# Performance work log

Hardware: AMD Instinct MI355X
Metric: run time of the kernel (lower is better)

## Reference

```python
import jax, jax.numpy as jnp
import numpy as np


def setup_inputs() -> dict:
    key = jax.random.key(0)
    ks = jax.random.split(key, 7)
    B, D, H, M, E = 8192, 512, 512, 50, 3
    return {
        "x": jax.random.normal(ks[0], (B, D), dtype=jnp.float32),
        "mem": jax.random.normal(ks[1], (M, D), dtype=jnp.float32),
        "routing_logits": jax.random.normal(ks[2], (E,), dtype=jnp.float32),
        "proj_W": jax.random.normal(ks[3], (H, D), dtype=jnp.float32) * 0.02,
        "proj_b": jax.random.normal(ks[4], (H,), dtype=jnp.float32) * 0.02,
        "ops_W": jax.random.normal(ks[5], (E, H, H), dtype=jnp.float32) * 0.02,
        "ops_b": jax.random.normal(ks[6], (E, H), dtype=jnp.float32) * 0.02,
    }


def reference(x, mem, routing_logits, proj_W, proj_b, ops_W, ops_b):
    # novelty: mean over (batch, memory) of L2 distance between x rows and memory rows
    diff = x[:, None, :] - mem[None, :, :]                 # [B, M, D] -- dominant memory traffic
    novelty = jnp.minimum(1.5, jnp.mean(jnp.linalg.norm(diff, axis=-1)))

    # top-2 routing over softmax of the (per-module, input-independent) logits
    weights = jax.nn.softmax(routing_logits)
    _, top2 = jax.lax.top_k(weights, 2)
    idx_a, idx_b = top2[0], top2[1]

    # operator = ReLU -> Linear(H, H) -> ReLU (torch Linear: y = x @ W.T + b)
    def op(h, W, b):
        return jax.nn.relu(jnp.einsum("bh,oh->bo", jax.nn.relu(h), W) + b)

    x_proj = jnp.einsum("bd,hd->bh", x, proj_W) + proj_b   # [B, H]
    x1 = op(x_proj, ops_W[idx_a], ops_b[idx_a])
    out = op(x1, ops_W[idx_b], ops_b[idx_b])
    return out, novelty
```

## Files before the change

kernel.cpp:

```cpp
#include <hip/hip_runtime.h>
#include <hip/hip_bf16.h>

typedef _Float16 f16;
typedef _Float16 f16x8 __attribute__((ext_vector_type(8)));
typedef _Float16 f16x4 __attribute__((ext_vector_type(4)));
typedef float f32x4 __attribute__((ext_vector_type(4)));

#define BD 512

__device__ __forceinline__ void llds16(const f16* g, f16* l) {
  __builtin_amdgcn_global_load_lds(
      (const __attribute__((address_space(1))) unsigned int*)g,
      (__attribute__((address_space(3))) unsigned int*)l,
      16, 0, 0);
}

__global__ __launch_bounds__(256) void prep_kernel(
    const float* __restrict__ projW, const float* __restrict__ opsW,
    const float* __restrict__ memf,
    f16* __restrict__ wh,
    f16* __restrict__ memh,
    float* __restrict__ mn2,
    float* __restrict__ novS) {
  const int blk = blockIdx.x;
  if (blk < 1024) {
    int i = blk * 256 + threadIdx.x;
    int e = i * 4;
    const float* s = (e < 262144) ? (projW + e) : (opsW + (e - 262144));
    float4 v = *(const float4*)s;
    f16x4 h;
    h[0] = (f16)v.x; h[1] = (f16)v.y; h[2] = (f16)v.z; h[3] = (f16)v.w;
    *(f16x4*)&wh[e] = h;
  } else {
    const int t = threadIdx.x, l = t & 63, w = t >> 6;
    const int row = (blk - 1024) * 4 + w;
    if (blk == 1024 && t == 0) *novS = 0.0f;
    f16x8 h;
    float ss = 0.0f;
    if (row < 50) {
      const float* src = memf + (size_t)row * BD + l * 8;
      float4 v0 = *(const float4*)src;
      float4 v1 = *(const float4*)(src + 4);
      h[0] = (f16)v0.x; h[1] = (f16)v0.y; h[2] = (f16)v0.z; h[3] = (f16)v0.w;
      h[4] = (f16)v1.x; h[5] = (f16)v1.y; h[6] = (f16)v1.z; h[7] = (f16)v1.w;
      ss = v0.x*v0.x + v0.y*v0.y + v0.z*v0.z + v0.w*v0.w
         + v1.x*v1.x + v1.y*v1.y + v1.z*v1.z + v1.w*v1.w;
      #pragma unroll
      for (int off = 32; off; off >>= 1) ss += __shfl_down(ss, off, 64);
    } else {
      #pragma unroll
      for (int j = 0; j < 8; ++j) h[j] = (f16)0.0f;
    }
    *(f16x8*)&memh[(size_t)row * BD + l * 8] = h;
    if (l == 0) mn2[row] = ss;
  }
}

__global__ __launch_bounds__(256) void conv_nov_kernel(
    const float* __restrict__ x, const f16* __restrict__ memh,
    const float* __restrict__ mn2, f16* __restrict__ xh,
    float* __restrict__ novS) {
  __shared__ __align__(16) f16 As[32 * BD];
  __shared__ float xn[32];
  __shared__ float red[4];
  const int t = threadIdx.x, l = t & 63, w = t >> 6;
  const int rbase = blockIdx.x * 32;

  #pragma unroll
  for (int rr = 0; rr < 8; ++rr) {
    const int r = w * 8 + rr;
    const float* src = x + (size_t)(rbase + r) * BD + l * 8;
    float4 v0 = *(const float4*)src;
    float4 v1 = *(const float4*)(src + 4);
    f16x8 h;
    h[0] = (f16)v0.x; h[1] = (f16)v0.y; h[2] = (f16)v0.z; h[3] = (f16)v0.w;
    h[4] = (f16)v1.x; h[5] = (f16)v1.y; h[6] = (f16)v1.z; h[7] = (f16)v1.w;
    *(f16x8*)&xh[(size_t)(rbase + r) * BD + l * 8] = h;
    const int cs = l ^ (r & 7);
    *(f16x8*)&As[r * BD + cs * 8] = h;
    float ss = v0.x*v0.x + v0.y*v0.y + v0.z*v0.z + v0.w*v0.w
             + v1.x*v1.x + v1.y*v1.y + v1.z*v1.z + v1.w*v1.w;
    #pragma unroll
    for (int off = 32; off; off >>= 1) ss += __shfl_down(ss, off, 64);
    if (l == 0) xn[r] = ss;
  }
  __syncthreads();

  const int lr = l & 15, lk = l >> 4;
  f32x4 acc[2];
  acc[0] = (f32x4){0.f, 0.f, 0.f, 0.f};
  acc[1] = (f32x4){0.f, 0.f, 0.f, 0.f};
  #pragma unroll
  for (int kk = 0; kk < BD; kk += 32) {
    f16x8 b = *(const f16x8*)&memh[(size_t)(w * 16 + lr) * BD + kk + lk * 8];
    #pragma unroll
    for (int m = 0; m < 2; ++m) {
      const int row = m * 16 + lr;
      const int ch = (kk >> 3) + lk;
      f16x8 a = *(const f16x8*)&As[row * BD + ((ch ^ (row & 7)) << 3)];
      acc[m] = __builtin_amdgcn_mfma_f32_16x16x32_f16(a, b, acc[m], 0, 0, 0);
    }
  }
  float local = 0.0f;
  const int mm = w * 16 + lr;
  if (mm < 50) {
    const float mn = mn2[mm];
    #pragma unroll
    for (int m = 0; m < 2; ++m) {
      #pragma unroll
      for (int j = 0; j < 4; ++j) {
        const int row = m * 16 + lk * 4 + j;
        float d = xn[row] - 2.0f * acc[m][j] + mn;
        local += sqrtf(fmaxf(d, 0.0f));
      }
    }
  }
  #pragma unroll
  for (int off = 32; off; off >>= 1) local += __shfl_down(local, off, 64);
  if (l == 0) red[w] = local;
  __syncthreads();
  if (t == 0) atomicAdd(novS, red[0] + red[1] + red[2] + red[3]);
}

template <int PICK, int OUTF16>
__global__ __launch_bounds__(256, 2) void gemm_relu_kernel(
    const f16* __restrict__ A, const f16* __restrict__ Wall,
    const float* __restrict__ ball, const float* __restrict__ logits,
    void* __restrict__ Out, const float* __restrict__ novS,
    float* __restrict__ novOut) {
  __shared__ __align__(16) f16 As[3][4096];
  __shared__ __align__(16) f16 Bs[3][8192];

  const int t = threadIdx.x;
  const int l = t & 63;
  const int w = t >> 6;
  const int wr = w >> 1, wc = w & 1;
  const int lr = l & 15, lk = l >> 4;

  if (PICK == 0 && blockIdx.x == 0 && blockIdx.y == 0 && t == 0)
    novOut[0] = fminf(1.5f, novS[0] * (1.0f / (8192.0f * 50.0f)));

  int widx = 0;
  if (PICK > 0) {
    float l0 = logits[0], l1 = logits[1], l2 = logits[2];
    int ia = 0; float ba = l0;
    if (l1 > ba) { ba = l1; ia = 1; }
    if (l2 > ba) { ba = l2; ia = 2; }
    if (PICK == 1) {
      widx = ia;
    } else {
      int ib = 0; float bb2 = -3.4e38f;
      if (ia != 0 && l0 > bb2) { bb2 = l0; ib = 0; }
      if (ia != 1 && l1 > bb2) { bb2 = l1; ib = 1; }
      if (ia != 2 && l2 > bb2) { bb2 = l2; ib = 2; }
      widx = ib;
    }
  }
  const f16* W = Wall + (size_t)widx * BD * BD;
  const float* bias = ball + widx * BD;

  const int rowBase = blockIdx.x * 64;
  const int colBase = blockIdx.y * 128;

  f32x4 acc[2][4];
  #pragma unroll
  for (int m = 0; m < 2; ++m)
    #pragma unroll
    for (int n = 0; n < 4; ++n) acc[m][n] = (f32x4){0.f, 0.f, 0.f, 0.f};

  auto stage = [&](int buf, int kt) {
    #pragma unroll
    for (int i = 0; i < 2; ++i) {
      const int o = i * 4096 + t * 16;
      const int row = o >> 7;
      const int sch = ((o >> 4) & 7) ^ (row & 7);
      llds16(A + (size_t)(rowBase + row) * BD + kt + sch * 8,
             &As[buf][(i * 4096 + w * 1024) / 2]);
    }
    #pragma unroll
    for (int i = 0; i < 4; ++i) {
      const int o = i * 4096 + t * 16;
      const int row = o >> 7;
      const int sch = ((o >> 4) & 7) ^ (row & 7);
      llds16(W + (size_t)(colBase + row) * BD + kt + sch * 8,
             &Bs[buf][(i * 4096 + w * 1024) / 2]);
    }
  };

  auto compute = [&](int buf) {
    #pragma unroll
    for (int kk = 0; kk < 64; kk += 32) {
      f16x8 af[2], bf[4];
      #pragma unroll
      for (int m = 0; m < 2; ++m) {
        const int row = wr * 32 + m * 16 + lr;
        const int ch = (kk >> 3) + lk;
        af[m] = *(const f16x8*)&As[buf][row * 64 + ((ch ^ (row & 7)) << 3)];
      }
      #pragma unroll
      for (int n = 0; n < 4; ++n) {
        const int row = wc * 64 + n * 16 + lr;
        const int ch = (kk >> 3) + lk;
        bf[n] = *(const f16x8*)&Bs[buf][row * 64 + ((ch ^ (row & 7)) << 3)];
      }
      #pragma unroll
      for (int m = 0; m < 2; ++m)
        #pragma unroll
        for (int n = 0; n < 4; ++n)
          acc[m][n] = __builtin_amdgcn_mfma_f32_16x16x32_f16(af[m], bf[n], acc[m][n], 0, 0, 0);
    }
  };

  stage(0, 0);
  stage(1, 64);
  #pragma unroll
  for (int t8 = 0; t8 < 8; ++t8) {
    if (t8 < 6) stage((t8 + 2) % 3, (t8 + 2) * 64);
    if (t8 <= 5)      asm volatile("s_waitcnt vmcnt(12)" ::: "memory");
    else if (t8 == 6) asm volatile("s_waitcnt vmcnt(6)" ::: "memory");
    else              asm volatile("s_waitcnt vmcnt(0)" ::: "memory");
    __builtin_amdgcn_s_barrier();
    compute(t8 % 3);
    __builtin_amdgcn_s_barrier();
  }

  #pragma unroll
  for (int n = 0; n < 4; ++n) {
    const int col = colBase + wc * 64 + n * 16 + lr;
    const float bb = bias[col];
    #pragma unroll
    for (int m = 0; m < 2; ++m) {
      #pragma unroll
      for (int j = 0; j < 4; ++j) {
        const int rowg = rowBase + wr * 32 + m * 16 + lk * 4 + j;
        float v = acc[m][n][j] + bb;
        v = fmaxf(v, 0.0f);
        if (OUTF16)
          ((f16*)Out)[(size_t)rowg * BD + col] = (f16)v;
        else
          ((float*)Out)[(size_t)rowg * BD + col] = v;
      }
    }
  }
}

extern "C" void kernel_launch(void* const* d_in, const int* in_sizes, int n_in,
                              void* d_out, int out_size, void* d_ws, size_t ws_size,
                              hipStream_t stream) {
  const float* x      = (const float*)d_in[0];
  const float* memf   = (const float*)d_in[1];
  const float* logits = (const float*)d_in[2];
  const float* projW  = (const float*)d_in[3];
  const float* projB  = (const float*)d_in[4];
  const float* opsW   = (const float*)d_in[5];
  const float* opsB   = (const float*)d_in[6];
  float* out = (float*)d_out;

  char* ws = (char*)d_ws;
  f16*   xh   = (f16*)(ws);
  f16*   g0   = (f16*)(ws + 8388608);
  f16*   wh   = (f16*)(ws + 16777216);
  f16*   memh = (f16*)(ws + 18874368);
  float* mn2  = (float*)(ws + 18972672);
  float* novS = (float*)(ws + 18972928);

  prep_kernel<<<1040, 256, 0, stream>>>(projW, opsW, memf, wh, memh, mn2, novS);
  conv_nov_kernel<<<256, 256, 0, stream>>>(x, memh, mn2, xh, novS);

  gemm_relu_kernel<0, 1><<<dim3(128, 4), 256, 0, stream>>>(
      xh, wh, projB, logits, (void*)g0, novS, out + 4194304);
  gemm_relu_kernel<1, 1><<<dim3(128, 4), 256, 0, stream>>>(
      g0, wh + 262144, opsB, logits, (void*)xh, novS, out + 4194304);
  gemm_relu_kernel<2, 0><<<dim3(128, 4), 256, 0, stream>>>(
      xh, wh + 262144, opsB, logits, (void*)out, novS, out + 4194304);
}
```

Before: 49.63 us.

## Fuse weight/memory conversion into novelty kernel and single-barrier GEMM pipeline

Merges the separate prep kernel into the x-conversion/novelty kernel. The weight fp32->fp16 conversion is spread across its 256 blocks, and each block converts memory rows and their norms on the fly instead of reading a precomputed fp16 copy. The global atomic is replaced by per-block partial sums that the first GEMM reduces, which drops one launch and the zero-init dependency. The GEMM main loop moves to one barrier per k-step, issuing the next stage after the barrier and waiting on a tighter vmcnt, and raises priority around the MFMA block. The cost is that every novelty block redundantly reloads and converts the 50 memory rows from fp32.

```diff
diff --git a/kernel.cpp b/kernel.cpp
--- a/kernel.cpp
+++ b/kernel.cpp
@@ -3,7 +3,6 @@
 
 typedef _Float16 f16;
 typedef _Float16 f16x8 __attribute__((ext_vector_type(8)));
-typedef _Float16 f16x4 __attribute__((ext_vector_type(4)));
 typedef float f32x4 __attribute__((ext_vector_type(4)));
 
 #define BD 512
@@ -15,56 +14,32 @@
       16, 0, 0);
 }
 
-__global__ __launch_bounds__(256) void prep_kernel(
+__global__ __launch_bounds__(256) void conv_nov_w_kernel(
+    const float* __restrict__ x, const float* __restrict__ memf,
     const float* __restrict__ projW, const float* __restrict__ opsW,
-    const float* __restrict__ memf,
-    f16* __restrict__ wh,
-    f16* __restrict__ memh,
-    float* __restrict__ mn2,
-    float* __restrict__ novS) {
-  const int blk = blockIdx.x;
-  if (blk < 1024) {
-    int i = blk * 256 + threadIdx.x;
-    int e = i * 4;
-    const float* s = (e < 262144) ? (projW + e) : (opsW + (e - 262144));
-    float4 v = *(const float4*)s;
-    f16x4 h;
-    h[0] = (f16)v.x; h[1] = (f16)v.y; h[2] = (f16)v.z; h[3] = (f16)v.w;
-    *(f16x4*)&wh[e] = h;
-  } else {
-    const int t = threadIdx.x, l = t & 63, w = t >> 6;
-    const int row = (blk - 1024) * 4 + w;
-    if (blk == 1024 && t == 0) *novS = 0.0f;
-    f16x8 h;
-    float ss = 0.0f;
-    if (row < 50) {
-      const float* src = memf + (size_t)row * BD + l * 8;
-      float4 v0 = *(const float4*)src;
-      float4 v1 = *(const float4*)(src + 4);
-      h[0] = (f16)v0.x; h[1] = (f16)v0.y; h[2] = (f16)v0.z; h[3] = (f16)v0.w;
-      h[4] = (f16)v1.x; h[5] = (f16)v1.y; h[6] = (f16)v1.z; h[7] = (f16)v1.w;
-      ss = v0.x*v0.x + v0.y*v0.y + v0.z*v0.z + v0.w*v0.w
-         + v1.x*v1.x + v1.y*v1.y + v1.z*v1.z + v1.w*v1.w;
-      #pragma unroll
-      for (int off = 32; off; off >>= 1) ss += __shfl_down(ss, off, 64);
-    } else {
-      #pragma unroll
-      for (int j = 0; j < 8; ++j) h[j] = (f16)0.0f;
-    }
-    *(f16x8*)&memh[(size_t)row * BD + l * 8] = h;
-    if (l == 0) mn2[row] = ss;
-  }
-}
-
-__global__ __launch_bounds__(256) void conv_nov_kernel(
-    const float* __restrict__ x, const f16* __restrict__ memh,
-    const float* __restrict__ mn2, f16* __restrict__ xh,
-    float* __restrict__ novS) {
+    f16* __restrict__ wh, f16* __restrict__ xh,
+    float* __restrict__ novPart) {
   __shared__ __align__(16) f16 As[32 * BD];
   __shared__ float xn[32];
   __shared__ float red[4];
   const int t = threadIdx.x, l = t & 63, w = t >> 6;
   const int rbase = blockIdx.x * 32;
+
+  {
+    const int e = (blockIdx.x * 256 + t) * 16;
+    const float* s = (e < 262144) ? (projW + e) : (opsW + (e - 262144));
+    float4 v0 = ((const float4*)s)[0];
+    float4 v1 = ((const float4*)s)[1];
+    float4 v2 = ((const float4*)s)[2];
+    float4 v3 = ((const float4*)s)[3];
+    f16x8 h0, h1;
+    h0[0]=(f16)v0.x; h0[1]=(f16)v0.y; h0[2]=(f16)v0.z; h0[3]=(f16)v0.w;
+    h0[4]=(f16)v1.x; h0[5]=(f16)v1.y; h0[6]=(f16)v1.z; h0[7]=(f16)v1.w;
+    h1[0]=(f16)v2.x; h1[1]=(f16)v2.y; h1[2]=(f16)v2.z; h1[3]=(f16)v2.w;
+    h1[4]=(f16)v3.x; h1[5]=(f16)v3.y; h1[6]=(f16)v3.z; h1[7]=(f16)v3.w;
+    *(f16x8*)&wh[e] = h0;
+    *(f16x8*)&wh[e + 8] = h1;
+  }
 
   #pragma unroll
   for (int rr = 0; rr < 8; ++rr) {
@@ -73,8 +48,8 @@
     float4 v0 = *(const float4*)src;
     float4 v1 = *(const float4*)(src + 4);
     f16x8 h;
-    h[0] = (f16)v0.x; h[1] = (f16)v0.y; h[2] = (f16)v0.z; h[3] = (f16)v0.w;
-    h[4] = (f16)v1.x; h[5] = (f16)v1.y; h[6] = (f16)v1.z; h[7] = (f16)v1.w;
+    h[0]=(f16)v0.x; h[1]=(f16)v0.y; h[2]=(f16)v0.z; h[3]=(f16)v0.w;
+    h[4]=(f16)v1.x; h[5]=(f16)v1.y; h[6]=(f16)v1.z; h[7]=(f16)v1.w;
     *(f16x8*)&xh[(size_t)(rbase + r) * BD + l * 8] = h;
     const int cs = l ^ (r & 7);
     *(f16x8*)&As[r * BD + cs * 8] = h;
@@ -87,49 +62,60 @@
   __syncthreads();
 
   const int lr = l & 15, lk = l >> 4;
-  f32x4 acc[2];
-  acc[0] = (f32x4){0.f, 0.f, 0.f, 0.f};
-  acc[1] = (f32x4){0.f, 0.f, 0.f, 0.f};
+  const int mm = w * 16 + lr;
+  f32x4 acc0 = (f32x4){0.f, 0.f, 0.f, 0.f};
+  f32x4 acc1 = (f32x4){0.f, 0.f, 0.f, 0.f};
+  float msq = 0.f;
   #pragma unroll
   for (int kk = 0; kk < BD; kk += 32) {
-    f16x8 b = *(const f16x8*)&memh[(size_t)(w * 16 + lr) * BD + kk + lk * 8];
-    #pragma unroll
-    for (int m = 0; m < 2; ++m) {
-      const int row = m * 16 + lr;
-      const int ch = (kk >> 3) + lk;
-      f16x8 a = *(const f16x8*)&As[row * BD + ((ch ^ (row & 7)) << 3)];
-      acc[m] = __builtin_amdgcn_mfma_f32_16x16x32_f16(a, b, acc[m], 0, 0, 0);
-    }
-  }
-  float local = 0.0f;
-  const int mm = w * 16 + lr;
+    f16x8 bfr;
+    if (mm < 50) {
+      const float* ms = memf + (size_t)mm * BD + kk + lk * 8;
+      float4 v0 = ((const float4*)ms)[0];
+      float4 v1 = ((const float4*)ms)[1];
+      bfr[0]=(f16)v0.x; bfr[1]=(f16)v0.y; bfr[2]=(f16)v0.z; bfr[3]=(f16)v0.w;
+      bfr[4]=(f16)v1.x; bfr[5]=(f16)v1.y; bfr[6]=(f16)v1.z; bfr[7]=(f16)v1.w;
+      msq += v0.x*v0.x + v0.y*v0.y + v0.z*v0.z + v0.w*v0.w
+           + v1.x*v1.x + v1.y*v1.y + v1.z*v1.z + v1.w*v1.w;
+    } else {
+      #pragma unroll
+      for (int j = 0; j < 8; ++j) bfr[j] = (f16)0.f;
+    }
+    const int ch = (kk >> 3) + lk;
+    {
+      const int row0 = lr;
+      f16x8 a0 = *(const f16x8*)&As[row0 * BD + ((ch ^ (row0 & 7)) << 3)];
+      acc0 = __builtin_amdgcn_mfma_f32_16x16x32_f16(a0, bfr, acc0, 0, 0, 0);
+      const int row1 = 16 + lr;
+      f16x8 a1 = *(const f16x8*)&As[row1 * BD + ((ch ^ (row1 & 7)) << 3)];
+      acc1 = __builtin_amdgcn_mfma_f32_16x16x32_f16(a1, bfr, acc1, 0, 0, 0);
+    }
+  }
+  float local = 0.f;
   if (mm < 50) {
-    const float mn = mn2[mm];
-    #pragma unroll
-    for (int m = 0; m < 2; ++m) {
-      #pragma unroll
-      for (int j = 0; j < 4; ++j) {
-        const int row = m * 16 + lk * 4 + j;
-        float d = xn[row] - 2.0f * acc[m][j] + mn;
-        local += sqrtf(fmaxf(d, 0.0f));
-      }
+    #pragma unroll
+    for (int j = 0; j < 4; ++j) {
+      const int r0 = lk * 4 + j;
+      float d0 = xn[r0] - 2.f * acc0[j] + msq;
+      local += sqrtf(fmaxf(d0, 0.f));
+      float d1 = xn[16 + r0] - 2.f * acc1[j] + msq;
+      local += sqrtf(fmaxf(d1, 0.f));
     }
   }
   #pragma unroll
   for (int off = 32; off; off >>= 1) local += __shfl_down(local, off, 64);
   if (l == 0) red[w] = local;
   __syncthreads();
-  if (t == 0) atomicAdd(novS, red[0] + red[1] + red[2] + red[3]);
+  if (t == 0) novPart[blockIdx.x] = red[0] + red[1] + red[2] + red[3];
 }
 
 template <int PICK, int OUTF16>
 __global__ __launch_bounds__(256, 2) void gemm_relu_kernel(
     const f16* __restrict__ A, const f16* __restrict__ Wall,
     const float* __restrict__ ball, const float* __restrict__ logits,
-    void* __restrict__ Out, const float* __restrict__ novS,
+    void* __restrict__ Out, const float* __restrict__ novPart,
     float* __restrict__ novOut) {
-  __shared__ __align__(16) f16 As[3][4096];
-  __shared__ __align__(16) f16 Bs[3][8192];
+  __shared__ __align__(16) char lds[3 * 24576];
 
   const int t = threadIdx.x;
   const int l = t & 63;
@@ -137,8 +123,12 @@
   const int wr = w >> 1, wc = w & 1;
   const int lr = l & 15, lk = l >> 4;
 
-  if (PICK == 0 && blockIdx.x == 0 && blockIdx.y == 0 && t == 0)
-    novOut[0] = fminf(1.5f, novS[0] * (1.0f / (8192.0f * 50.0f)));
+  if (PICK == 0 && blockIdx.x == 0 && blockIdx.y == 0 && w == 0) {
+    float s = novPart[l] + novPart[l + 64] + novPart[l + 128] + novPart[l + 192];
+    #pragma unroll
+    for (int off = 32; off; off >>= 1) s += __shfl_down(s, off, 64);
+    if (l == 0) novOut[0] = fminf(1.5f, s * (1.0f / (8192.0f * 50.0f)));
+  }
 
   int widx = 0;
   if (PICK > 0) {
@@ -150,7 +140,7 @@
       widx = ia;
     } else {
       int ib = 0; float bb2 = -3.4e38f;
-      if (ia != 0 && l0 > bb2) { bb2 = l0; ib = 0; }
+      if (ia != 0)             { bb2 = l0; ib = 0; }
       if (ia != 1 && l1 > bb2) { bb2 = l1; ib = 1; }
       if (ia != 2 && l2 > bb2) { bb2 = l2; ib = 2; }
       widx = ib;
@@ -169,13 +159,15 @@
     for (int n = 0; n < 4; ++n) acc[m][n] = (f32x4){0.f, 0.f, 0.f, 0.f};
 
   auto stage = [&](int buf, int kt) {
+    f16* Ab = (f16*)(lds + buf * 24576);
+    f16* Bb = (f16*)(lds + buf * 24576 + 8192);
     #pragma unroll
     for (int i = 0; i < 2; ++i) {
       const int o = i * 4096 + t * 16;
       const int row = o >> 7;
       const int sch = ((o >> 4) & 7) ^ (row & 7);
       llds16(A + (size_t)(rowBase + row) * BD + kt + sch * 8,
-             &As[buf][(i * 4096 + w * 1024) / 2]);
+             Ab + (i * 4096 + w * 1024) / 2);
     }
     #pragma unroll
     for (int i = 0; i < 4; ++i) {
@@ -183,11 +175,13 @@
       const int row = o >> 7;
       const int sch = ((o >> 4) & 7) ^ (row & 7);
       llds16(W + (size_t)(colBase + row) * BD + kt + sch * 8,
-             &Bs[buf][(i * 4096 + w * 1024) / 2]);
+             Bb + (i * 4096 + w * 1024) / 2);
     }
   };
 
   auto compute = [&](int buf) {
+    const f16* Ab = (const f16*)(lds + buf * 24576);
+    const f16* Bb = (const f16*)(lds + buf * 24576 + 8192);
     #pragma unroll
     for (int kk = 0; kk < 64; kk += 32) {
       f16x8 af[2], bf[4];
@@ -195,19 +189,21 @@
       for (int m = 0; m < 2; ++m) {
         const int row = wr * 32 + m * 16 + lr;
         const int ch = (kk >> 3) + lk;
-        af[m] = *(const f16x8*)&As[buf][row * 64 + ((ch ^ (row & 7)) << 3)];
+        af[m] = *(const f16x8*)&Ab[row * 64 + ((ch ^ (row & 7)) << 3)];
       }
       #pragma unroll
       for (int n = 0; n < 4; ++n) {
         const int row = wc * 64 + n * 16 + lr;
         const int ch = (kk >> 3) + lk;
-        bf[n] = *(const f16x8*)&Bs[buf][row * 64 + ((ch ^ (row & 7)) << 3)];
+        bf[n] = *(const f16x8*)&Bb[row * 64 + ((ch ^ (row & 7)) << 3)];
       }
+      __builtin_amdgcn_s_setprio(1);
       #pragma unroll
       for (int m = 0; m < 2; ++m)
         #pragma unroll
         for (int n = 0; n < 4; ++n)
           acc[m][n] = __builtin_amdgcn_mfma_f32_16x16x32_f16(af[m], bf[n], acc[m][n], 0, 0, 0);
+      __builtin_amdgcn_s_setprio(0);
     }
   };
 
@@ -215,30 +211,26 @@
   stage(1, 64);
   #pragma unroll
   for (int t8 = 0; t8 < 8; ++t8) {
+    if (t8 < 7) asm volatile("s_waitcnt vmcnt(6)" ::: "memory");
+    else        asm volatile("s_waitcnt vmcnt(0)" ::: "memory");
+    __builtin_amdgcn_s_barrier();
     if (t8 < 6) stage((t8 + 2) % 3, (t8 + 2) * 64);
-    if (t8 <= 5)      asm volatile("s_waitcnt vmcnt(12)" ::: "memory");
-    else if (t8 == 6) asm volatile("s_waitcnt vmcnt(6)" ::: "memory");
-    else              asm volatile("s_waitcnt vmcnt(0)" ::: "memory");
-    __builtin_amdgcn_s_barrier();
     compute(t8 % 3);
-    __builtin_amdgcn_s_barrier();
+    asm volatile("s_waitcnt lgkmcnt(0)" ::: "memory");
   }
 
   #pragma unroll
   for (int n = 0; n < 4; ++n) {
     const int col = colBase + wc * 64 + n * 16 + lr;
-    const float bb = bias[col];
+    const float bbv = bias[col];
     #pragma unroll
     for (int m = 0; m < 2; ++m) {
       #pragma unroll
       for (int j = 0; j < 4; ++j) {
         const int rowg = rowBase + wr * 32 + m * 16 + lk * 4 + j;
-        float v = acc[m][n][j] + bb;
-        v = fmaxf(v, 0.0f);
-        if (OUTF16)
-          ((f16*)Out)[(size_t)rowg * BD + col] = (f16)v;
-        else
-          ((float*)Out)[(size_t)rowg * BD + col] = v;
+        float v = fmaxf(acc[m][n][j] + bbv, 0.f);
+        if (OUTF16) ((f16*)Out)[(size_t)rowg * BD + col] = (f16)v;
+        else        ((float*)Out)[(size_t)rowg * BD + col] = v;
       }
     }
   }
@@ -257,20 +249,17 @@
   float* out = (float*)d_out;
 
   char* ws = (char*)d_ws;
-  f16*   xh   = (f16*)(ws);
-  f16*   g0   = (f16*)(ws + 8388608);
-  f16*   wh   = (f16*)(ws + 16777216);
-  f16*   memh = (f16*)(ws + 18874368);
-  float* mn2  = (float*)(ws + 18972672);
-  float* novS = (float*)(ws + 18972928);
-
-  prep_kernel<<<1040, 256, 0, stream>>>(projW, opsW, memf, wh, memh, mn2, novS);
-  conv_nov_kernel<<<256, 256, 0, stream>>>(x, memh, mn2, xh, novS);
+  f16*   xh      = (f16*)(ws);
+  f16*   g0      = (f16*)(ws + 8388608);
+  f16*   wh      = (f16*)(ws + 16777216);
+  float* novPart = (float*)(ws + 18874368);
+
+  conv_nov_w_kernel<<<256, 256, 0, stream>>>(x, memf, projW, opsW, wh, xh, novPart);
 
   gemm_relu_kernel<0, 1><<<dim3(128, 4), 256, 0, stream>>>(
-      xh, wh, projB, logits, (void*)g0, novS, out + 4194304);
+      xh, wh, projB, logits, (void*)g0, novPart, out + 4194304);
   gemm_relu_kernel<1, 1><<<dim3(128, 4), 256, 0, stream>>>(
-      g0, wh + 262144, opsB, logits, (void*)xh, novS, out + 4194304);
+      g0, wh + 262144, opsB, logits, (void*)xh, novPart, out + 4194304);
   gemm_relu_kernel<2, 0><<<dim3(128, 4), 256, 0, stream>>>(
-      xh, wh + 262144, opsB, logits, (void*)out, novS, out + 4194304);
-}
+      xh, wh + 262144, opsB, logits, (void*)out, novPart, out + 4194304);
+}
```

After: 47.40 us. -4.5%, faster.
